# Optimization experiments

Measured on AMD Instinct MI355X. Metric: run time of the kernel, lower is better.

The kernel has to match this reference:

```python
import jax, jax.numpy as jnp
import numpy as np
from jax import lax

N, C_IN, C_OUT, T, V = 16, 256, 256, 300, 25
K = 3            # s_kernel_size
TK = 9           # t_kernel_size
BN_EPS = 1e-5


def setup_inputs() -> dict:
    key = jax.random.key(0)
    ks = jax.random.split(key, 12)
    x = jax.random.normal(ks[0], (N, C_IN, T, V), dtype=jnp.float32)
    A = jax.random.uniform(ks[1], (K, V, V), dtype=jnp.float32)
    att_A = jax.random.uniform(ks[2], (N, 1, V, V), dtype=jnp.float32)  # unused by S_GC
    M = jnp.ones((K, V, V), dtype=jnp.float32)
    # 1x1 spatial conv: out = K*C_OUT channels
    conv_w = jax.random.normal(ks[3], (K * C_OUT, C_IN), dtype=jnp.float32) * 0.02
    conv_b = jnp.zeros((K * C_OUT,), dtype=jnp.float32)
    # BN1 (eval mode)
    bn1_gamma = jnp.ones((C_OUT,), dtype=jnp.float32)
    bn1_beta = jnp.zeros((C_OUT,), dtype=jnp.float32)
    bn1_mean = jax.random.normal(ks[4], (C_OUT,), dtype=jnp.float32) * 0.1
    bn1_var = jax.random.uniform(ks[5], (C_OUT,), dtype=jnp.float32) + 0.5
    # temporal conv: kernel (TK, 1), stride 1, pad ((TK-1)//2, 0)
    tconv_w = jax.random.normal(ks[6], (C_OUT, C_OUT, TK, 1), dtype=jnp.float32) * 0.02
    tconv_b = jnp.zeros((C_OUT,), dtype=jnp.float32)
    # BN2 (eval mode)
    bn2_gamma = jnp.ones((C_OUT,), dtype=jnp.float32)
    bn2_beta = jnp.zeros((C_OUT,), dtype=jnp.float32)
    bn2_mean = jax.random.normal(ks[7], (C_OUT,), dtype=jnp.float32) * 0.1
    bn2_var = jax.random.uniform(ks[8], (C_OUT,), dtype=jnp.float32) + 0.5
    return {
        "x": x, "A": A, "att_A": att_A, "M": M,
        "conv_w": conv_w, "conv_b": conv_b,
        "bn1_gamma": bn1_gamma, "bn1_beta": bn1_beta, "bn1_mean": bn1_mean, "bn1_var": bn1_var,
        "tconv_w": tconv_w, "tconv_b": tconv_b,
        "bn2_gamma": bn2_gamma, "bn2_beta": bn2_beta, "bn2_mean": bn2_mean, "bn2_var": bn2_var,
    }


def _bn(x, gamma, beta, mean, var):
    # eval-mode BatchNorm2d over channel dim of NCHW tensor
    scale = gamma / jnp.sqrt(var + BN_EPS)
    return x * scale[None, :, None, None] + (beta - mean * scale)[None, :, None, None]


def reference(x, A, att_A, M, conv_w, conv_b,
              bn1_gamma, bn1_beta, bn1_mean, bn1_var,
              tconv_w, tconv_b,
              bn2_gamma, bn2_beta, bn2_mean, bn2_var):
    # --- S_GC: 1x1 conv -> view (n,K,c,t,v) -> einsum with A*M ---
    y = jnp.einsum('nctv,oc->notv', x, conv_w) + conv_b[None, :, None, None]
    y = y.reshape(N, K, C_OUT, T, V)
    sgc = jnp.einsum('nkctv,kvw->nctw', y, A * M)
    # --- tgc: BN -> ReLU -> temporal conv -> BN -> Dropout(0) -> ReLU ---
    h = jax.nn.relu(_bn(sgc, bn1_gamma, bn1_beta, bn1_mean, bn1_var))
    h = lax.conv_general_dilated(
        h, tconv_w, window_strides=(1, 1),
        padding=(((TK - 1) // 2, (TK - 1) // 2), (0, 0)),
        dimension_numbers=('NCHW', 'OIHW', 'NCHW'))
    h = h + tconv_b[None, :, None, None]
    h = jax.nn.relu(_bn(h, bn2_gamma, bn2_beta, bn2_mean, bn2_var))
    # --- residual: identity (in_channels == out_channels, stride == 1) ---
    return h + x
```

## Files before the change

### kernel.cpp

```cpp
#include <hip/hip_runtime.h>
#include <math.h>

constexpr int TVL = 7500;
constexpr int CIN = 256;
constexpr int CO  = 256;
constexpr int KO  = 768;
constexpr int KK3 = 2304;
#define BNEPS 1e-5f

typedef __attribute__((ext_vector_type(8))) short short8;
typedef __attribute__((ext_vector_type(4))) float f32x4;
typedef unsigned short ushortT;

static __device__ __forceinline__ ushortT f2bf(float v) {
    unsigned x = __float_as_uint(v);
    unsigned r = (x + 0x7fffu + ((x >> 16) & 1u)) >> 16;
    return (ushortT)r;
}
static __device__ __forceinline__ float bf2f(ushortT u) {
    return __uint_as_float((unsigned)u << 16);
}

static __device__ __forceinline__ void gll16(const void* g, void* l) {
    __builtin_amdgcn_global_load_lds(
        (const __attribute__((address_space(1))) void*)g,
        (__attribute__((address_space(3))) void*)l, 16, 0, 0);
}

static __device__ __forceinline__ void xcd_remap(int gx, int gy,
                                                 int& bx, int& by, int& bz)
{
    const int gz = gridDim.z;
    const int total = gx * gy * gz;
    const int lin = blockIdx.x + gx * (blockIdx.y + gy * blockIdx.z);
    const int q = total >> 3, r = total & 7;
    const int xcd = lin & 7, idx = lin >> 3;
    const int nl = (xcd < r ? xcd * (q + 1) : r * (q + 1) + (xcd - r) * q) + idx;
    bx = nl % gx;
    const int rest = nl / gx;
    by = rest % gy;
    bz = rest / gy;
}

__global__ void ksplit_w1(const float* __restrict__ w,
                          ushortT* __restrict__ dH, ushortT* __restrict__ dL,
                          ushortT* __restrict__ zb)
{
    if (blockIdx.x == 0 && threadIdx.x < 128) zb[threadIdx.x] = 0;
    int i = blockIdx.x * 256 + threadIdx.x;
    if (i < KO * CIN) {
        float v = w[i];
        ushortT h = f2bf(v);
        dH[i] = h;
        dL[i] = f2bf(v - bf2f(h));
    }
}

__global__ void ksplit_w3(const float* __restrict__ w,
                          ushortT* __restrict__ dH, ushortT* __restrict__ dL)
{
    int i = blockIdx.x * 256 + threadIdx.x;
    if (i < CO * KK3) {
        int o = i / KK3, rem = i - o * KK3;
        int c = rem / 9, dt = rem - c * 9;
        float v = w[i];
        ushortT h = f2bf(v);
        int j = o * KK3 + dt * 256 + c;
        dH[j] = h;
        dL[j] = f2bf(v - bf2f(h));
    }
}

__global__ __launch_bounds__(256) void ktrans_split(
    const float* __restrict__ src, size_t zstr,
    ushortT* __restrict__ dH, ushortT* __restrict__ dL)
{
    __shared__ float tile[32][33];
    const int z = blockIdx.z;
    src += (size_t)z * zstr;
    dH  += (size_t)z * TVL * 256;
    dL  += (size_t)z * TVL * 256;
    const int tx = threadIdx.x & 31, ty = threadIdx.x >> 5;
    const int wBase = blockIdx.x * 32, cBase = blockIdx.y * 32;
    #pragma unroll
    for (int i = 0; i < 4; ++i) {
        int r = ty + i * 8;
        int w = wBase + tx;
        tile[r][tx] = (w < TVL) ? src[(size_t)(cBase + r) * TVL + w] : 0.f;
    }
    __syncthreads();
    #pragma unroll
    for (int i = 0; i < 4; ++i) {
        int wr = ty + i * 8;
        int w = wBase + wr;
        if (w < TVL) {
            float v = tile[tx][wr];
            ushortT hi = f2bf(v);
            ushortT lo = f2bf(v - bf2f(hi));
            dH[(size_t)w * 256 + cBase + tx] = hi;
            dL[(size_t)w * 256 + cBase + tx] = lo;
        }
    }
}

__global__ __launch_bounds__(256, 3) void k1_mfma(
    const ushortT* __restrict__ Wh, const ushortT* __restrict__ Wl,
    const ushortT* __restrict__ Xh, const ushortT* __restrict__ Xl,
    const ushortT* __restrict__ zb,
    const float* __restrict__ bias, float* __restrict__ out1)
{
    __shared__ __align__(16) short Bh[2][4096], Bl[2][4096];
    const int tid = threadIdx.x;
    int bx, by, bz;
    xcd_remap(gridDim.x, gridDim.y, bx, by, bz);
    const int ng = bz;
    const int rowBase = by * 128;
    const int colBase = bx * 128;
    const ushortT* XhN = Xh + (size_t)ng * TVL * 256;
    const ushortT* XlN = Xl + (size_t)ng * TVL * 256;

    f32x4 acc[4][4];
    #pragma unroll
    for (int a = 0; a < 4; ++a)
        #pragma unroll
        for (int b = 0; b < 4; ++b) acc[a][b] = (f32x4){0.f, 0.f, 0.f, 0.f};

    const int r0 = tid >> 2, s = tid & 3;
    const int wv = tid >> 6, lane = tid & 63;
    const int wy = wv >> 1, wx = wv & 1;
    const int q = lane >> 4, l15 = lane & 15;
    const int qs0 = s ^ ((r0 >> 1) & 3);
    const int ldo0 = tid * 16, ldo1 = 4096 + tid * 16;
    const int bcol0 = colBase + r0, bcol1 = colBase + r0 + 64;

    const ushortT* WhR = Wh + (size_t)(rowBase + wy * 64 + l15) * CIN + q * 8;
    const ushortT* WlR = Wl + (size_t)(rowBase + wy * 64 + l15) * CIN + q * 8;

    auto stageB = [&](int kk, int p) {
        short* bhp = Bh[p]; short* blp = Bl[p];
        const size_t goB0 = (size_t)bcol0 * 256 + kk + qs0 * 8;
        const size_t goB1 = (size_t)bcol1 * 256 + kk + qs0 * 8;
        gll16(bcol0 < TVL ? (const void*)(XhN + goB0) : (const void*)zb, (char*)bhp + ldo0);
        gll16(bcol0 < TVL ? (const void*)(XlN + goB0) : (const void*)zb, (char*)blp + ldo0);
        gll16(bcol1 < TVL ? (const void*)(XhN + goB1) : (const void*)zb, (char*)bhp + ldo1);
        gll16(bcol1 < TVL ? (const void*)(XlN + goB1) : (const void*)zb, (char*)blp + ldo1);
    };
    auto loadA = [&](int kk, short8* dh, short8* dl) {
        #pragma unroll
        for (int mi = 0; mi < 4; ++mi) {
            dh[mi] = *(const short8*)(WhR + (size_t)mi * 16 * CIN + kk);
            dl[mi] = *(const short8*)(WlR + (size_t)mi * 16 * CIN + kk);
        }
    };

    short8 cAh[4], cAl[4], nAh[4], nAl[4];
    loadA(0, cAh, cAl);
    stageB(0, 0);
    __syncthreads();
    int p = 0;

    #pragma unroll 1
    for (int kk = 0; kk < CIN; kk += 32) {
        const bool more = (kk + 32 < CIN);
        if (more) {
            loadA(kk + 32, nAh, nAl);
            stageB(kk + 32, p ^ 1);
        }

        const char* BhP = (const char*)Bh[p];
        const char* BlP = (const char*)Bl[p];
        #pragma unroll
        for (int ni = 0; ni < 4; ++ni) {
            const int scn = wx * 64 + ni * 16 + l15;
            const int off = scn * 64 + ((q ^ ((scn >> 1) & 3)) << 4);
            const short8 bh = *(const short8*)(BhP + off);
            const short8 bl = *(const short8*)(BlP + off);
            #pragma unroll
            for (int mi = 0; mi < 4; ++mi) {
                acc[mi][ni] = __builtin_amdgcn_mfma_f32_16x16x32_bf16(cAh[mi], bh, acc[mi][ni], 0, 0, 0);
                acc[mi][ni] = __builtin_amdgcn_mfma_f32_16x16x32_bf16(cAh[mi], bl, acc[mi][ni], 0, 0, 0);
                acc[mi][ni] = __builtin_amdgcn_mfma_f32_16x16x32_bf16(cAl[mi], bh, acc[mi][ni], 0, 0, 0);
            }
        }
        __syncthreads();
        p ^= 1;
        if (more) {
            #pragma unroll
            for (int i = 0; i < 4; ++i) { cAh[i] = nAh[i]; cAl[i] = nAl[i]; }
        }
    }

    float* out1n = out1 + (size_t)ng * KO * TVL;
    #pragma unroll
    for (int mi = 0; mi < 4; ++mi)
        #pragma unroll
        for (int rr = 0; rr < 4; ++rr) {
            const int row = rowBase + wy * 64 + mi * 16 + q * 4 + rr;
            const float bv = bias[row];
            #pragma unroll
            for (int ni = 0; ni < 4; ++ni) {
                const int col = colBase + wx * 64 + ni * 16 + l15;
                if (col < TVL)
                    out1n[(size_t)row * TVL + col] = acc[mi][ni][rr] + bv;
            }
        }
}

__global__ __launch_bounds__(256) void k2_sgc(
    const float* out1, const float* __restrict__ A,
    const float* __restrict__ Mm, const float* __restrict__ g1,
    const float* __restrict__ b1, const float* __restrict__ m1,
    const float* __restrict__ v1, float* h)
{
    __shared__ __align__(16) float AMs[3 * 25 * 28];
    const int tid = threadIdx.x;
    for (int i = tid; i < 1875; i += 256)
        AMs[(i / 25) * 28 + (i % 25)] = A[i] * Mm[i];
    __syncthreads();

    const int r  = blockIdx.x * 256 + tid;
    const int t2 = r % 150;
    const int rc = r / 150;
    const int c  = rc & 255;
    const int ng = rc >> 8;
    const int t  = t2 * 2;

    const float* base = out1 + ((size_t)ng * KO + c) * TVL + t * 25;
    float o0[25], o1[25];
    #pragma unroll
    for (int w = 0; w < 25; ++w) { o0[w] = 0.f; o1[w] = 0.f; }

    for (int k = 0; k < 3; ++k) {
        const float* yp = base + (size_t)k * CO * TVL;
        float y0[25], y1[25];
        #pragma unroll
        for (int v = 0; v < 25; ++v) { y0[v] = yp[v]; y1[v] = yp[25 + v]; }
        const float* amk = &AMs[k * 25 * 28];
        for (int v = 0; v < 25; ++v) {
            const float* am = amk + v * 28;
            const float ya = y0[v], yb = y1[v];
            #pragma unroll
            for (int w = 0; w < 25; ++w) {
                const float a = am[w];
                o0[w] += ya * a;
                o1[w] += yb * a;
            }
        }
    }

    const float sc = g1[c] / sqrtf(v1[c] + BNEPS);
    const float bi = b1[c] - m1[c] * sc;
    float* hp = h + ((size_t)ng * KO + c) * TVL + t * 25;
    #pragma unroll
    for (int w = 0; w < 25; ++w) {
        const float va = o0[w] * sc + bi;
        const float vb = o1[w] * sc + bi;
        hp[w]      = va > 0.f ? va : 0.f;
        hp[25 + w] = vb > 0.f ? vb : 0.f;
    }
}

__global__ __launch_bounds__(256, 3) void k3_mfma(
    const ushortT* __restrict__ Wh, const ushortT* __restrict__ Wl,
    const ushortT* __restrict__ Hh, const ushortT* __restrict__ Hl,
    const ushortT* __restrict__ zb,
    const float* __restrict__ tb, const float* __restrict__ g2,
    const float* __restrict__ b2, const float* __restrict__ m2,
    const float* __restrict__ v2, const float* __restrict__ x,
    float* __restrict__ out, int n0)
{
    __shared__ __align__(16) short Sh[384 * 32], Sl[384 * 32];
    const int tid = threadIdx.x;
    int bx, by, bz;
    xcd_remap(gridDim.x, gridDim.y, bx, by, bz);
    const int ng = bz;
    const int rowBase = by * 128;
    const int colBase = bx * 128;
    const ushortT* HhN = Hh + (size_t)ng * TVL * 256;
    const ushortT* HlN = Hl + (size_t)ng * TVL * 256;

    f32x4 acc[4][4];
    #pragma unroll
    for (int a = 0; a < 4; ++a)
        #pragma unroll
        for (int b = 0; b < 4; ++b) acc[a][b] = (f32x4){0.f, 0.f, 0.f, 0.f};

    const int r0 = tid >> 2, s = tid & 3;
    const int wv = tid >> 6, lane = tid & 63;
    const int wy = wv >> 1, wx = wv & 1;
    const int q = lane >> 4, l15 = lane & 15;
    const int qs0 = s ^ ((r0 >> 1) & 3);

    const ushortT* WhR = Wh + (size_t)(rowBase + wy * 64 + l15) * KK3 + q * 8;
    const ushortT* WlR = Wl + (size_t)(rowBase + wy * 64 + l15) * KK3 + q * 8;

    auto stageStrip = [&](int c0) {
        #pragma unroll
        for (int i = 0; i < 6; ++i) {
            const int gcol = colBase - 128 + i * 64 + r0;
            const bool ok = (unsigned)gcol < (unsigned)TVL;
            const size_t go = (size_t)gcol * 256 + c0 + qs0 * 8;
            gll16(ok ? (const void*)(HhN + go) : (const void*)zb,
                  (char*)Sh + i * 4096 + tid * 16);
            gll16(ok ? (const void*)(HlN + go) : (const void*)zb,
                  (char*)Sl + i * 4096 + tid * 16);
        }
    };
    auto loadA = [&](int kp, short8* dh, short8* dl) {
        #pragma unroll
        for (int mi = 0; mi < 4; ++mi) {
            dh[mi] = *(const short8*)(WhR + (size_t)mi * 16 * KK3 + kp);
            dl[mi] = *(const short8*)(WlR + (size_t)mi * 16 * KK3 + kp);
        }
    };

    short8 cAh[4], cAl[4], nAh[4], nAl[4];
    loadA(0, cAh, cAl);

    #pragma unroll 1
    for (int cc = 0; cc < 8; ++cc) {
        const int c0 = cc * 32;
        if (cc) __syncthreads();
        stageStrip(c0);
        __syncthreads();

        #pragma unroll 1
        for (int dt = 0; dt < 9; ++dt) {
            int ndt = dt + 1, nc0 = c0;
            if (ndt == 9) { ndt = 0; nc0 += 32; }
            const bool hasNext = (nc0 < 256);
            if (hasNext) loadA(ndt * 256 + nc0, nAh, nAl);

            const int sbase = wx * 64 + dt * 25 + 28;
            #pragma unroll
            for (int ni = 0; ni < 4; ++ni) {
                const int sc = sbase + ni * 16 + l15;
                const int off = sc * 64 + ((q ^ ((sc >> 1) & 3)) << 4);
                const short8 bh = *(const short8*)((const char*)Sh + off);
                const short8 bl = *(const short8*)((const char*)Sl + off);
                #pragma unroll
                for (int mi = 0; mi < 4; ++mi) {
                    acc[mi][ni] = __builtin_amdgcn_mfma_f32_16x16x32_bf16(cAh[mi], bh, acc[mi][ni], 0, 0, 0);
                    acc[mi][ni] = __builtin_amdgcn_mfma_f32_16x16x32_bf16(cAh[mi], bl, acc[mi][ni], 0, 0, 0);
                    acc[mi][ni] = __builtin_amdgcn_mfma_f32_16x16x32_bf16(cAl[mi], bh, acc[mi][ni], 0, 0, 0);
                }
            }
            if (hasNext) {
                #pragma unroll
                for (int i = 0; i < 4; ++i) { cAh[i] = nAh[i]; cAl[i] = nAl[i]; }
            }
        }
    }

    const float* xn = x   + (size_t)(n0 + ng) * CO * TVL;
    float*       on = out + (size_t)(n0 + ng) * CO * TVL;
    #pragma unroll
    for (int mi = 0; mi < 4; ++mi)
        #pragma unroll
        for (int rr = 0; rr < 4; ++rr) {
            const int row = rowBase + wy * 64 + mi * 16 + q * 4 + rr;
            const float sc = g2[row] / sqrtf(v2[row] + BNEPS);
            const float bb = (tb[row] - m2[row]) * sc + b2[row];
            #pragma unroll
            for (int ni = 0; ni < 4; ++ni) {
                const int col = colBase + wx * 64 + ni * 16 + l15;
                if (col < TVL) {
                    const size_t o = (size_t)row * TVL + col;
                    on[o] = fmaxf(acc[mi][ni][rr] * sc + bb, 0.f) + xn[o];
                }
            }
        }
}

extern "C" void kernel_launch(void* const* d_in, const int* in_sizes, int n_in,
                              void* d_out, int out_size, void* d_ws, size_t ws_size,
                              hipStream_t stream)
{
    const float* x  = (const float*)d_in[0];
    const float* A  = (const float*)d_in[1];
    const float* Mm = (const float*)d_in[3];
    const float* cw = (const float*)d_in[4];
    const float* cb = (const float*)d_in[5];
    const float* g1 = (const float*)d_in[6];
    const float* b1 = (const float*)d_in[7];
    const float* m1 = (const float*)d_in[8];
    const float* v1 = (const float*)d_in[9];
    const float* tw = (const float*)d_in[10];
    const float* tb = (const float*)d_in[11];
    const float* g2 = (const float*)d_in[12];
    const float* b2 = (const float*)d_in[13];
    const float* m2 = (const float*)d_in[14];
    const float* v2 = (const float*)d_in[15];
    float* out = (float*)d_out;

    ushortT* zb  = (ushortT*)d_ws;
    ushortT* W1h = (ushortT*)((char*)d_ws + 256);
    ushortT* W1l = W1h + KO * CIN;
    ushortT* W3h = W1l + KO * CIN;
    ushortT* W3l = W3h + CO * KK3;
    char* dyn = (char*)(W3l + CO * KK3);
    const size_t fixed = (size_t)(dyn - (char*)d_ws);
    const size_t avail = ws_size > fixed ? ws_size - fixed : 0;
    const size_t perN = (size_t)KO * TVL * 4 + 2 * (size_t)TVL * 256 * 2;
    int g = 16;
    while (g > 1 && (size_t)g * perN > avail) g >>= 1;

    float*   out1 = (float*)dyn;
    ushortT* Xh   = (ushortT*)(out1 + (size_t)g * KO * TVL);
    ushortT* Xl   = Xh + (size_t)g * TVL * 256;

    hipLaunchKernelGGL(ksplit_w1, dim3((KO * CIN + 255) / 256), dim3(256), 0, stream, cw, W1h, W1l, zb);
    hipLaunchKernelGGL(ksplit_w3, dim3((CO * KK3 + 255) / 256), dim3(256), 0, stream, tw, W3h, W3l);

    for (int n0 = 0; n0 < 16; n0 += g) {
        hipLaunchKernelGGL(ktrans_split, dim3(235, 8, g), dim3(256), 0, stream,
                           x + (size_t)n0 * CIN * TVL, (size_t)CIN * TVL, Xh, Xl);
        hipLaunchKernelGGL(k1_mfma, dim3(59, 6, g), dim3(256), 0, stream,
                           W1h, W1l, Xh, Xl, zb, cb, out1);
        hipLaunchKernelGGL(k2_sgc, dim3(g * 150), dim3(256), 0, stream,
                           out1, A, Mm, g1, b1, m1, v1, out1 );
        hipLaunchKernelGGL(ktrans_split, dim3(235, 8, g), dim3(256), 0, stream,
                           out1, (size_t)KO * TVL, Xh, Xl);
        hipLaunchKernelGGL(k3_mfma, dim3(59, 2, g), dim3(256), 0, stream,
                           W3h, W3l, Xh, Xl, zb, tb, g2, b2, m2, v2, x, out, n0);
    }
}
```

Measured before the change: 1.435 ms.

## Stage temporal-conv weights through double-buffered LDS and raise MFMA wave priority

In the temporal-conv GEMM kernel, the weight (A) operand was loaded directly from global memory into registers by each wave. It is now staged into double-buffered, swizzled LDS tiles with async global-to-LDS loads, and each wave reads its fragments from there. A barrier is added after every dt step, and the occupancy hint in launch bounds is dropped. s_setprio is raised around the MFMA blocks in both GEMM kernels so compute waves get issue priority. The aim is to cut redundant global weight loads and register pressure, at the cost of more LDS use and extra synchronization per step.

```diff
diff --git a/kernel.cpp b/kernel.cpp
--- a/kernel.cpp
+++ b/kernel.cpp
@@ -169,6 +169,7 @@
 
         const char* BhP = (const char*)Bh[p];
         const char* BlP = (const char*)Bl[p];
+        __builtin_amdgcn_s_setprio(1);
         #pragma unroll
         for (int ni = 0; ni < 4; ++ni) {
             const int scn = wx * 64 + ni * 16 + l15;
@@ -182,6 +183,7 @@
                 acc[mi][ni] = __builtin_amdgcn_mfma_f32_16x16x32_bf16(cAl[mi], bh, acc[mi][ni], 0, 0, 0);
             }
         }
+        __builtin_amdgcn_s_setprio(0);
         __syncthreads();
         p ^= 1;
         if (more) {
@@ -260,7 +262,7 @@
     }
 }
 
-__global__ __launch_bounds__(256, 3) void k3_mfma(
+__global__ __launch_bounds__(256) void k3_mfma(
     const ushortT* __restrict__ Wh, const ushortT* __restrict__ Wl,
     const ushortT* __restrict__ Hh, const ushortT* __restrict__ Hl,
     const ushortT* __restrict__ zb,
@@ -270,6 +272,7 @@
     float* __restrict__ out, int n0)
 {
     __shared__ __align__(16) short Sh[384 * 32], Sl[384 * 32];
+    __shared__ __align__(16) short Ah[2][4096], Al[2][4096];
     const int tid = threadIdx.x;
     int bx, by, bz;
     xcd_remap(gridDim.x, gridDim.y, bx, by, bz);
@@ -290,9 +293,8 @@
     const int wy = wv >> 1, wx = wv & 1;
     const int q = lane >> 4, l15 = lane & 15;
     const int qs0 = s ^ ((r0 >> 1) & 3);
-
-    const ushortT* WhR = Wh + (size_t)(rowBase + wy * 64 + l15) * KK3 + q * 8;
-    const ushortT* WlR = Wl + (size_t)(rowBase + wy * 64 + l15) * KK3 + q * 8;
+    const int qsr = q ^ ((l15 >> 1) & 3);
+    const int ldo0 = tid * 16, ldo1 = 4096 + tid * 16;
 
     auto stageStrip = [&](int c0) {
         #pragma unroll
@@ -306,16 +308,17 @@
                   (char*)Sl + i * 4096 + tid * 16);
         }
     };
-    auto loadA = [&](int kp, short8* dh, short8* dl) {
-        #pragma unroll
-        for (int mi = 0; mi < 4; ++mi) {
-            dh[mi] = *(const short8*)(WhR + (size_t)mi * 16 * KK3 + kp);
-            dl[mi] = *(const short8*)(WlR + (size_t)mi * 16 * KK3 + kp);
-        }
+    auto stageA = [&](int kp, int p) {
+        short* ahp = Ah[p]; short* alp = Al[p];
+        const size_t goA = (size_t)(rowBase + r0) * KK3 + kp + qs0 * 8;
+        gll16(Wh + goA, (char*)ahp + ldo0);
+        gll16(Wl + goA, (char*)alp + ldo0);
+        gll16(Wh + goA + (size_t)64 * KK3, (char*)ahp + ldo1);
+        gll16(Wl + goA + (size_t)64 * KK3, (char*)alp + ldo1);
     };
 
-    short8 cAh[4], cAl[4], nAh[4], nAl[4];
-    loadA(0, cAh, cAl);
+    stageA(0, 0);
+    int p = 0;
 
     #pragma unroll 1
     for (int cc = 0; cc < 8; ++cc) {
@@ -328,10 +331,19 @@
         for (int dt = 0; dt < 9; ++dt) {
             int ndt = dt + 1, nc0 = c0;
             if (ndt == 9) { ndt = 0; nc0 += 32; }
-            const bool hasNext = (nc0 < 256);
-            if (hasNext) loadA(ndt * 256 + nc0, nAh, nAl);
-
+            if (nc0 < 256) stageA(ndt * 256 + nc0, p ^ 1);
+
+            const char* AhP = (const char*)Ah[p];
+            const char* AlP = (const char*)Al[p];
+            short8 ah[4], al[4];
+            #pragma unroll
+            for (int mi = 0; mi < 4; ++mi) {
+                const int off = (wy * 64 + mi * 16 + l15) * 64 + qsr * 16;
+                ah[mi] = *(const short8*)(AhP + off);
+                al[mi] = *(const short8*)(AlP + off);
+            }
             const int sbase = wx * 64 + dt * 25 + 28;
+            __builtin_amdgcn_s_setprio(1);
             #pragma unroll
             for (int ni = 0; ni < 4; ++ni) {
                 const int sc = sbase + ni * 16 + l15;
@@ -340,15 +352,14 @@
                 const short8 bl = *(const short8*)((const char*)Sl + off);
                 #pragma unroll
                 for (int mi = 0; mi < 4; ++mi) {
-                    acc[mi][ni] = __builtin_amdgcn_mfma_f32_16x16x32_bf16(cAh[mi], bh, acc[mi][ni], 0, 0, 0);
-                    acc[mi][ni] = __builtin_amdgcn_mfma_f32_16x16x32_bf16(cAh[mi], bl, acc[mi][ni], 0, 0, 0);
-                    acc[mi][ni] = __builtin_amdgcn_mfma_f32_16x16x32_bf16(cAl[mi], bh, acc[mi][ni], 0, 0, 0);
+                    acc[mi][ni] = __builtin_amdgcn_mfma_f32_16x16x32_bf16(ah[mi], bh, acc[mi][ni], 0, 0, 0);
+                    acc[mi][ni] = __builtin_amdgcn_mfma_f32_16x16x32_bf16(ah[mi], bl, acc[mi][ni], 0, 0, 0);
+                    acc[mi][ni] = __builtin_amdgcn_mfma_f32_16x16x32_bf16(al[mi], bh, acc[mi][ni], 0, 0, 0);
                 }
             }
-            if (hasNext) {
-                #pragma unroll
-                for (int i = 0; i < 4; ++i) { cAh[i] = nAh[i]; cAl[i] = nAl[i]; }
-            }
+            __builtin_amdgcn_s_setprio(0);
+            __syncthreads();
+            p ^= 1;
         }
     }
 
```

Result: faster. 1.254 ms (-12.6%).
